# Kernel tuning notes

Hardware: AMD Instinct MI355X
Metric: run time of the kernel (lower is better)

The kernel has to match this reference:

```python
import jax, jax.numpy as jnp
import numpy as np

SIGMA = 1e-4   # SoftRas coverage sharpness
GAMMA = 0.1    # depth-softmax temperature
IMAGE_SIZE = 128


def _normalize(v):
    return v / (jnp.linalg.norm(v, axis=-1, keepdims=True) + 1e-8)


def _look_at(eye, center, up):
    z = _normalize(eye - center)
    x = _normalize(jnp.cross(up, z))
    y = jnp.cross(z, x)
    R = jnp.stack([x, y, z], axis=-2)                       # (B,3,3)
    t = -jnp.einsum('bij,bj->bi', R, eye)
    B = eye.shape[0]
    M = jnp.tile(jnp.eye(4, dtype=eye.dtype), (B, 1, 1))
    M = M.at[:, :3, :3].set(R).at[:, :3, 3].set(t)
    return M


def _perspective(fov_y, aspect, near, far):
    f = 1.0 / np.tan(fov_y / 2.0)
    M = np.zeros((4, 4), np.float32)
    M[0, 0] = f / aspect
    M[1, 1] = f
    M[2, 2] = (far + near) / (near - far)
    M[2, 3] = 2.0 * far * near / (near - far)
    M[3, 2] = -1.0
    return jnp.asarray(M)


def _project(verts_world, eye, center, up):
    B, V, _ = verts_world.shape
    view = _look_at(eye, center, up)
    proj = _perspective(np.deg2rad(60.0), 1.0, 0.1, 10.0)
    M = jnp.einsum('ij,bjk->bik', proj, view)
    vh = jnp.concatenate([verts_world, jnp.ones((B, V, 1), verts_world.dtype)], -1)
    clip = jnp.einsum('bij,bvj->bvi', M, vh)
    return clip[..., :3] / (clip[..., 3:4] + 1e-8)            # (B,V,3) NDC


def _edge_dist(p, a, b):
    # p: (H,W,2); a,b: (B,F,2) -> unsigned point-to-segment distance (B,F,H,W)
    pa = p[None, None] - a[:, :, None, None]                  # (B,F,H,W,2)
    ba = (b - a)[:, :, None, None]                            # (B,F,1,1,2)
    t = jnp.clip(jnp.sum(pa * ba, -1) / (jnp.sum(ba * ba, -1) + 1e-12), 0.0, 1.0)
    d = pa - t[..., None] * ba
    return jnp.sqrt(jnp.sum(d * d, -1) + 1e-12)


def _cross2(u, v):
    return u[..., 0] * v[..., 1] - u[..., 1] * v[..., 0]


def _rasterize(verts_ndc, faces, colors, image_size):
    tri = verts_ndc[:, faces]                                 # (B,F,3,3)
    v2, vz = tri[..., :2], tri[..., 2]                        # (B,F,3,2), (B,F,3)
    xs = (jnp.arange(image_size) + 0.5) / image_size * 2.0 - 1.0
    ys = 1.0 - (jnp.arange(image_size) + 0.5) / image_size * 2.0
    X, Y = jnp.meshgrid(xs, ys, indexing='xy')
    p = jnp.stack([X, Y], -1)                                 # (H,W,2)

    a0, a1, a2 = v2[:, :, 0], v2[:, :, 1], v2[:, :, 2]        # (B,F,2)
    area = _cross2(a1 - a0, a2 - a0)[:, :, None, None]        # (B,F,1,1)
    denom = area + jnp.where(area >= 0, 1e-12, -1e-12)
    w0 = _cross2((a2 - a1)[:, :, None, None], p[None, None] - a1[:, :, None, None])
    w1 = _cross2((a0 - a2)[:, :, None, None], p[None, None] - a2[:, :, None, None])
    w2 = _cross2((a1 - a0)[:, :, None, None], p[None, None] - a0[:, :, None, None])
    b0, b1, b2 = w0 / denom, w1 / denom, w2 / denom           # barycentrics (B,F,H,W)
    inside = (b0 >= 0) & (b1 >= 0) & (b2 >= 0)

    d = jnp.minimum(jnp.minimum(_edge_dist(p, a0, a1), _edge_dist(p, a1, a2)),
                    _edge_dist(p, a2, a0))
    sgn = jnp.where(inside, 1.0, -1.0)
    prob = jax.nn.sigmoid(sgn * d * d / SIGMA)                # soft coverage (B,F,H,W)
    sil = 1.0 - jnp.prod(1.0 - prob, axis=1, keepdims=True)   # (B,1,H,W)

    bc0, bc1, bc2 = (jnp.clip(b0, 0., 1.), jnp.clip(b1, 0., 1.), jnp.clip(b2, 0., 1.))
    s = bc0 + bc1 + bc2 + 1e-8
    zpix = (bc0 * vz[:, :, 0, None, None] + bc1 * vz[:, :, 1, None, None]
            + bc2 * vz[:, :, 2, None, None]) / s
    zn = jnp.clip((1.0 - zpix) * 0.5, 0.0, 1.0)               # 1 = near
    m = jnp.max(zn, axis=1, keepdims=True)
    Dw = prob * jnp.exp((zn - m) / GAMMA)
    w_bg = jnp.exp((0.0 - m) / GAMMA)                         # background (far, black)
    Wn = Dw / (jnp.sum(Dw, axis=1, keepdims=True) + w_bg)     # (B,F,H,W)
    face_col = jnp.mean(colors[:, faces], axis=2)             # (B,F,3)
    rgb = jnp.einsum('bfhw,bfc->bchw', Wn, face_col)          # (B,3,H,W)
    return sil, rgb


def setup_inputs() -> dict:
    key = jax.random.key(0)
    k1, k2, k3, k4 = jax.random.split(key, 4)
    B, V, F = 4, 256, 256
    verts_world = jax.random.normal(k1, (B, V, 3), jnp.float32) * 0.5
    faces = jax.random.randint(k2, (F, 3), 0, V)
    colors = jax.random.uniform(k3, (B, V, 3), jnp.float32)
    eye = jnp.tile(jnp.array([0.0, 0.0, 2.5], jnp.float32), (B, 1)) \
          + jax.random.normal(k4, (B, 3), jnp.float32) * 0.05
    return {"verts_world": verts_world, "faces": faces, "colors": colors, "eye": eye}


def reference(verts_world, faces, colors, eye):
    B = verts_world.shape[0]
    center = jnp.zeros((B, 3), verts_world.dtype)
    up = jnp.tile(jnp.array([0.0, 1.0, 0.0], verts_world.dtype), (B, 1))
    verts_ndc = _project(verts_world, eye, center, up)
    return _rasterize(verts_ndc, faces, colors, IMAGE_SIZE)
```

## Files before the change

### kernel.cpp

```cpp
#include <hip/hip_runtime.h>

#define NB 4
#define NV 256
#define NF 256
#define IMG 128
#define STRIDE 60

typedef float v2f __attribute__((ext_vector_type(2)));

__device__ __forceinline__ float rcpf(float x) { return __builtin_amdgcn_rcpf(x); }
__device__ __forceinline__ float med01(float x) { return __builtin_amdgcn_fmed3f(x, 0.0f, 1.0f); }
__device__ __forceinline__ v2f fma2(v2f a, v2f b, v2f c) { return __builtin_elementwise_fma(a, b, c); }


__global__ void prep_faces(const float* __restrict__ verts,
                           const int* __restrict__ faces,
                           const float* __restrict__ colors,
                           const float* __restrict__ eye,
                           float* __restrict__ fd)
{
    int gid = blockIdx.x * blockDim.x + threadIdx.x;
    if (gid >= NB * NF) return;
    int b = gid >> 8;
    int f = gid & 255;

    const float fpj = 1.7320508075688772f;
    const float p22 = -1.0202020202020203f;
    const float p23 = -0.20202020202020202f;

    float ex = eye[b*3+0], ey = eye[b*3+1], ez = eye[b*3+2];
    float en  = sqrtf(ex*ex + ey*ey + ez*ez);
    float izn = 1.0f / (en + 1e-8f);
    float zx = ex*izn, zy = ey*izn, zz = ez*izn;
    float cn  = sqrtf(zz*zz + zx*zx);
    float ixn = 1.0f / (cn + 1e-8f);
    float xx = zz*ixn, xy = 0.0f, xz = -zx*ixn;
    float yx = zy*xz - zz*xy;
    float yy = zz*xx - zx*xz;
    float yz = zx*xy - zy*xx;
    float tx = -(xx*ex + xy*ey + xz*ez);
    float ty = -(yx*ex + yy*ey + yz*ez);
    float tz = -(zx*ex + zy*ey + zz*ez);

    int i0 = faces[f*3+0], i1 = faces[f*3+1], i2 = faces[f*3+2];
    int idx[3] = { i0, i1, i2 };

    float ax[3], ay[3], az[3];
#pragma unroll
    for (int k = 0; k < 3; ++k) {
        const float* v = verts + (b*NV + idx[k])*3;
        float vx = v[0], vy = v[1], vz = v[2];
        float cx  = fpj*(xx*vx + xy*vy + xz*vz + tx);
        float cyv = fpj*(yx*vx + yy*vy + yz*vz + ty);
        float zv  = zx*vx + zy*vy + zz*vz + tz;
        float cz  = p22*zv + p23;
        float cw  = -zv;
        float iw  = 1.0f / (cw + 1e-8f);
        ax[k] = cx*iw; ay[k] = cyv*iw; az[k] = cz*iw;
    }

    float a0x = ax[0], a0y = ay[0];
    float a1x = ax[1], a1y = ay[1];
    float a2x = ax[2], a2y = ay[2];

    float e01x = a1x - a0x, e01y = a1y - a0y;
    float e12x = a2x - a1x, e12y = a2y - a1y;
    float e20x = a0x - a2x, e20y = a0y - a2y;

    float area  = e01x*(a2y - a0y) - e01y*(a2x - a0x);
    float denom = area + (area >= 0.0f ? 1e-12f : -1e-12f);
    float idn   = 1.0f / denom;

    float A0 = -e12y*idn, B0 = e12x*idn, C0 = (e12y*a1x - e12x*a1y)*idn;
    float A1 = -e20y*idn, B1 = e20x*idn, C1 = (e20y*a2x - e20x*a2y)*idn;
    float A2 = -e01y*idn, B2 = e01x*idn, C2 = (e01y*a0x - e01x*a0y)*idn;

    float ib01 = 1.0f / (e01x*e01x + e01y*e01y + 1e-12f);
    float ib12 = 1.0f / (e12x*e12x + e12y*e12y + 1e-12f);
    float ib20 = 1.0f / (e20x*e20x + e20y*e20y + 1e-12f);

    const float third = (1.0f/3.0f);
    float cr = (colors[(b*NV+i0)*3+0] + colors[(b*NV+i1)*3+0] + colors[(b*NV+i2)*3+0]) * third;
    float cg = (colors[(b*NV+i0)*3+1] + colors[(b*NV+i1)*3+1] + colors[(b*NV+i2)*3+1]) * third;
    float cb = (colors[(b*NV+i0)*3+2] + colors[(b*NV+i1)*3+2] + colors[(b*NV+i2)*3+2]) * third;

    float* o = fd + (b*128 + (f >> 1))*STRIDE + (f & 1);
    o[ 0]=A0;   o[ 2]=B0;   o[ 4]=C0;
    o[ 6]=A1;   o[ 8]=B1;   o[10]=C1;
    o[12]=A2;   o[14]=B2;   o[16]=C2;
    o[18]=a0x;  o[20]=a0y;
    o[22]=e01x; o[24]=e01y; o[26]=e12x; o[28]=e12y; o[30]=e20x; o[32]=e20y;
    o[34]=e01x*ib01; o[36]=e01y*ib01;
    o[38]=e12x*ib12; o[40]=e12y*ib12;
    o[42]=e20x*ib20; o[44]=e20y*ib20;
    o[46]=az[0]; o[48]=az[1]; o[50]=az[2];
    o[52]=cr;   o[54]=cg;   o[56]=cb;
}

__launch_bounds__(512)
__global__ void raster(const float* __restrict__ fd, float* __restrict__ out)
{
    __shared__ float sP[8][64], sS[8][64];
    __shared__ float sR0[8][64], sR1[8][64], sR2[8][64];

    const int t   = threadIdx.x;
    const int cy  = threadIdx.y;
    const int b   = blockIdx.x >> 8;
    const int grp = blockIdx.x & 255;
    const int pixb = grp*64 + t;
    const int h = pixb >> 7;
    const int w = pixb & 127;

    const float px = (w + 0.5f) * (1.0f/64.0f) - 1.0f;
    const float py = 1.0f - (h + 0.5f) * (1.0f/64.0f);
    const v2f px2 = { px, px };
    const v2f py2 = { py, py };

    int foff = (b*128 + cy*16) * STRIDE;
    foff = __builtin_amdgcn_readfirstlane(foff);
    const float* fc = fd + foff;

    const float KSIG = 14426.950408889634f;
    const float KGAM = 14.426950408889634f;
    const v2f KSIG2 = { KSIG, KSIG };
    const v2f KGAM2 = { KGAM, KGAM };
    const v2f ONE2  = { 1.0f, 1.0f };
    const v2f NHALF = { -0.5f, -0.5f };
    const v2f HALF  = { 0.5f, 0.5f };
    const v2f EPS2  = { 1e-8f, 1e-8f };

    v2f prod2 = { 1.0f, 1.0f };
    v2f S2  = { 0.0f, 0.0f };
    v2f R02 = { 0.0f, 0.0f };
    v2f R12 = { 0.0f, 0.0f };
    v2f R22 = { 0.0f, 0.0f };

    for (int i = 0; i < 16; ++i) {
        const float* c = fc + i*STRIDE;
#define LD(k) (*(const v2f*)(c + 2*(k)))
        v2f A0 = LD(0),  B0 = LD(1),  C0 = LD(2);
        v2f A1 = LD(3),  B1 = LD(4),  C1 = LD(5);
        v2f A2 = LD(6),  B2 = LD(7),  C2 = LD(8);
        v2f a0x = LD(9), a0y = LD(10);
        v2f e01x = LD(11), e01y = LD(12);
        v2f e12x = LD(13), e12y = LD(14);
        v2f e20x = LD(15), e20y = LD(16);
        v2f g01x = LD(17), g01y = LD(18);
        v2f g12x = LD(19), g12y = LD(20);
        v2f g20x = LD(21), g20y = LD(22);
        v2f z0 = LD(23), z1 = LD(24), z2 = LD(25);
        v2f cr = LD(26), cg = LD(27), cb = LD(28);
#undef LD

        v2f b0 = fma2(A0, px2, B0*py2) + C0;
        v2f b1 = fma2(A1, px2, B1*py2) + C1;
        v2f b2 = fma2(A2, px2, B2*py2) + C2;

        v2f pa0x = px2 - a0x, pa0y = py2 - a0y;
        v2f pa1x = pa0x - e01x, pa1y = pa0y - e01y;
        v2f pa2x = pa0x + e20x, pa2y = pa0y + e20y;

        v2f tt = fma2(pa0x, g01x, pa0y*g01y);
        tt = (v2f){ med01(tt.x), med01(tt.y) };
        v2f dx = fma2(-tt, e01x, pa0x);
        v2f dy = fma2(-tt, e01y, pa0y);
        v2f dd0 = fma2(dx, dx, dy*dy);
        tt = fma2(pa1x, g12x, pa1y*g12y);
        tt = (v2f){ med01(tt.x), med01(tt.y) };
        dx = fma2(-tt, e12x, pa1x);
        dy = fma2(-tt, e12y, pa1y);
        v2f dd1 = fma2(dx, dx, dy*dy);
        tt = fma2(pa2x, g20x, pa2y*g20y);
        tt = (v2f){ med01(tt.x), med01(tt.y) };
        dx = fma2(-tt, e20x, pa2x);
        dy = fma2(-tt, e20y, pa2y);
        v2f dd2 = fma2(dx, dx, dy*dy);

        float ddl = fminf(fminf(dd0.x, dd1.x), dd2.x);
        float ddh = fminf(fminf(dd0.y, dd1.y), dd2.y);
        v2f ddk = ((v2f){ ddl, ddh }) * KSIG2;

        float inl = fminf(fminf(b0.x, b1.x), b2.x);
        float inh = fminf(fminf(b0.y, b1.y), b2.y);
        float qx = (inl >= 0.0f) ? -ddk.x : ddk.x;
        float qy = (inh >= 0.0f) ? -ddk.y : ddk.y;

        v2f e2 = { exp2f(qx), exp2f(qy) };
        v2f den = e2 + ONE2;
        v2f prob = { rcpf(den.x), rcpf(den.y) };

        prod2 = fma2(-prob, prod2, prod2);

        v2f bc0 = { med01(b0.x), med01(b0.y) };
        v2f bc1 = { med01(b1.x), med01(b1.y) };
        v2f bc2 = { med01(b2.x), med01(b2.y) };
        v2f s   = (bc0 + bc1) + (bc2 + EPS2);
        v2f zs  = fma2(bc0, z0, fma2(bc1, z1, bc2*z2));
        v2f irs = { rcpf(s.x), rcpf(s.y) };
        v2f zp  = zs * irs;
        v2f zn  = fma2(zp, NHALF, HALF);
        zn = (v2f){ med01(zn.x), med01(zn.y) };

        v2f znk = zn * KGAM2;
        v2f ez  = { exp2f(znk.x), exp2f(znk.y) };
        v2f wgt = prob * ez;

        S2  = S2 + wgt;
        R02 = fma2(wgt, cr, R02);
        R12 = fma2(wgt, cg, R12);
        R22 = fma2(wgt, cb, R22);
    }

    sP[cy][t]  = prod2.x * prod2.y;
    sS[cy][t]  = S2.x  + S2.y;
    sR0[cy][t] = R02.x + R02.y;
    sR1[cy][t] = R12.x + R12.y;
    sR2[cy][t] = R22.x + R22.y;
    __syncthreads();

    if (cy == 0) {
        float P  = 1.0f, St = 0.0f, r0 = 0.0f, r1 = 0.0f, r2 = 0.0f;
#pragma unroll
        for (int c2 = 0; c2 < 8; ++c2) {
            P  *= sP[c2][t];
            St += sS[c2][t];
            r0 += sR0[c2][t];
            r1 += sR1[c2][t];
            r2 += sR2[c2][t];
        }
        float iden = rcpf(St + 1.0f);

        out[b*16384 + pixb] = 1.0f - P;
        float* rgb = out + 65536;
        rgb[(b*3 + 0)*16384 + pixb] = r0 * iden;
        rgb[(b*3 + 1)*16384 + pixb] = r1 * iden;
        rgb[(b*3 + 2)*16384 + pixb] = r2 * iden;
    }
}

extern "C" void kernel_launch(void* const* d_in, const int* in_sizes, int n_in,
                              void* d_out, int out_size, void* d_ws, size_t ws_size,
                              hipStream_t stream)
{
    const float* verts  = (const float*)d_in[0];
    const int*   faces  = (const int*)d_in[1];
    const float* colors = (const float*)d_in[2];
    const float* eye    = (const float*)d_in[3];
    float* out = (float*)d_out;
    float* fd  = (float*)d_ws;

    hipLaunchKernelGGL(prep_faces, dim3(4), dim3(256), 0, stream,
                       verts, faces, colors, eye, fd);
    hipLaunchKernelGGL(raster, dim3(1024), dim3(64, 8), 0, stream, fd, out);
}
```

Before: 37.85 us.

## Fold sigma/gamma scaling into face data, use constant-address scalar loads

Prescales the edge and vertex data by sqrt(KSIG) in the prep kernel so the distance comes out already multiplied by the sigma constant, and folds the gamma scale into the depth-normalisation FMA and clamp. The inside test is rewritten as a max of negated barycentrics plus copysign, and the barycentric evaluation becomes a nested FMA. Face data is padded to stride 64 and read through the constant address space so the compiler can use scalar memory loads. It also switches to the raw hardware exp2 and adds unroll 2. Risks are small numerical differences from the prescaling and raw exp2, and changed edge behaviour where a barycentric is exactly zero.

```diff
diff --git a/kernel.cpp b/kernel.cpp
--- a/kernel.cpp
+++ b/kernel.cpp
@@ -4,12 +4,15 @@
 #define NV 256
 #define NF 256
 #define IMG 128
-#define STRIDE 60
+#define STRIDE 64
 
 typedef float v2f __attribute__((ext_vector_type(2)));
+#define CONST_AS __attribute__((address_space(4)))
 
 __device__ __forceinline__ float rcpf(float x) { return __builtin_amdgcn_rcpf(x); }
+__device__ __forceinline__ float ex2(float x)  { return __builtin_amdgcn_exp2f(x); }
 __device__ __forceinline__ float med01(float x) { return __builtin_amdgcn_fmed3f(x, 0.0f, 1.0f); }
+__device__ __forceinline__ v2f med01_2(v2f v) { return (v2f){ med01(v.x), med01(v.y) }; }
 __device__ __forceinline__ v2f fma2(v2f a, v2f b, v2f c) { return __builtin_elementwise_fma(a, b, c); }
 
 
@@ -27,6 +30,8 @@
     const float fpj = 1.7320508075688772f;
     const float p22 = -1.0202020202020203f;
     const float p23 = -0.20202020202020202f;
+    const float SC  = 120.11224139682566f;
+    const float ISC = 1.0f / 120.11224139682566f;
 
     float ex = eye[b*3+0], ey = eye[b*3+1], ez = eye[b*3+2];
     float en  = sqrtf(ex*ex + ey*ey + ez*ez);
@@ -88,11 +93,11 @@
     o[ 0]=A0;   o[ 2]=B0;   o[ 4]=C0;
     o[ 6]=A1;   o[ 8]=B1;   o[10]=C1;
     o[12]=A2;   o[14]=B2;   o[16]=C2;
-    o[18]=a0x;  o[20]=a0y;
-    o[22]=e01x; o[24]=e01y; o[26]=e12x; o[28]=e12y; o[30]=e20x; o[32]=e20y;
-    o[34]=e01x*ib01; o[36]=e01y*ib01;
-    o[38]=e12x*ib12; o[40]=e12y*ib12;
-    o[42]=e20x*ib20; o[44]=e20y*ib20;
+    o[18]=a0x*SC;  o[20]=a0y*SC;
+    o[22]=e01x*SC; o[24]=e01y*SC; o[26]=e12x*SC; o[28]=e12y*SC; o[30]=e20x*SC; o[32]=e20y*SC;
+    o[34]=e01x*ib01*ISC; o[36]=e01y*ib01*ISC;
+    o[38]=e12x*ib12*ISC; o[40]=e12y*ib12*ISC;
+    o[42]=e20x*ib20*ISC; o[44]=e20y*ib20*ISC;
     o[46]=az[0]; o[48]=az[1]; o[50]=az[2];
     o[52]=cr;   o[54]=cg;   o[56]=cb;
 }
@@ -113,21 +118,23 @@
 
     const float px = (w + 0.5f) * (1.0f/64.0f) - 1.0f;
     const float py = 1.0f - (h + 0.5f) * (1.0f/64.0f);
-    const v2f px2 = { px, px };
-    const v2f py2 = { py, py };
+    const float SC = 120.11224139682566f;
+    const v2f px2  = { px, px };
+    const v2f py2  = { py, py };
+    const v2f pxs2 = { px*SC, px*SC };
+    const v2f pys2 = { py*SC, py*SC };
+
+    const float KGAM = 14.426950408889634f;
+    const v2f KGH_NEG = { -0.5f*KGAM, -0.5f*KGAM };
+    const v2f KGH_POS = {  0.5f*KGAM,  0.5f*KGAM };
+    const v2f ONE2 = { 1.0f, 1.0f };
+    const v2f EPS2 = { 1e-8f, 1e-8f };
 
     int foff = (b*128 + cy*16) * STRIDE;
     foff = __builtin_amdgcn_readfirstlane(foff);
-    const float* fc = fd + foff;
-
-    const float KSIG = 14426.950408889634f;
-    const float KGAM = 14.426950408889634f;
-    const v2f KSIG2 = { KSIG, KSIG };
-    const v2f KGAM2 = { KGAM, KGAM };
-    const v2f ONE2  = { 1.0f, 1.0f };
-    const v2f NHALF = { -0.5f, -0.5f };
-    const v2f HALF  = { 0.5f, 0.5f };
-    const v2f EPS2  = { 1e-8f, 1e-8f };
+    const float* fda = (const float*)__builtin_assume_aligned(fd, 256);
+    const CONST_AS float* fc =
+        (const CONST_AS float*)(unsigned long long)(fda + foff);
 
     v2f prod2 = { 1.0f, 1.0f };
     v2f S2  = { 0.0f, 0.0f };
@@ -135,9 +142,10 @@
     v2f R12 = { 0.0f, 0.0f };
     v2f R22 = { 0.0f, 0.0f };
 
+#pragma unroll 2
     for (int i = 0; i < 16; ++i) {
-        const float* c = fc + i*STRIDE;
-#define LD(k) (*(const v2f*)(c + 2*(k)))
+        const CONST_AS float* c = fc + i*STRIDE;
+#define LD(k) (*(const CONST_AS v2f*)(c + 2*(k)))
         v2f A0 = LD(0),  B0 = LD(1),  C0 = LD(2);
         v2f A1 = LD(3),  B1 = LD(4),  C1 = LD(5);
         v2f A2 = LD(6),  B2 = LD(7),  C2 = LD(8);
@@ -152,57 +160,48 @@
         v2f cr = LD(26), cg = LD(27), cb = LD(28);
 #undef LD
 
-        v2f b0 = fma2(A0, px2, B0*py2) + C0;
-        v2f b1 = fma2(A1, px2, B1*py2) + C1;
-        v2f b2 = fma2(A2, px2, B2*py2) + C2;
-
-        v2f pa0x = px2 - a0x, pa0y = py2 - a0y;
+        v2f b0 = fma2(A0, px2, fma2(B0, py2, C0));
+        v2f b1 = fma2(A1, px2, fma2(B1, py2, C1));
+        v2f b2 = fma2(A2, px2, fma2(B2, py2, C2));
+
+        v2f pa0x = pxs2 - a0x, pa0y = pys2 - a0y;
         v2f pa1x = pa0x - e01x, pa1y = pa0y - e01y;
         v2f pa2x = pa0x + e20x, pa2y = pa0y + e20y;
 
-        v2f tt = fma2(pa0x, g01x, pa0y*g01y);
-        tt = (v2f){ med01(tt.x), med01(tt.y) };
+        v2f tt = med01_2(fma2(pa0x, g01x, pa0y*g01y));
         v2f dx = fma2(-tt, e01x, pa0x);
         v2f dy = fma2(-tt, e01y, pa0y);
         v2f dd0 = fma2(dx, dx, dy*dy);
-        tt = fma2(pa1x, g12x, pa1y*g12y);
-        tt = (v2f){ med01(tt.x), med01(tt.y) };
+        tt = med01_2(fma2(pa1x, g12x, pa1y*g12y));
         dx = fma2(-tt, e12x, pa1x);
         dy = fma2(-tt, e12y, pa1y);
         v2f dd1 = fma2(dx, dx, dy*dy);
-        tt = fma2(pa2x, g20x, pa2y*g20y);
-        tt = (v2f){ med01(tt.x), med01(tt.y) };
+        tt = med01_2(fma2(pa2x, g20x, pa2y*g20y));
         dx = fma2(-tt, e20x, pa2x);
         dy = fma2(-tt, e20y, pa2y);
         v2f dd2 = fma2(dx, dx, dy*dy);
 
         float ddl = fminf(fminf(dd0.x, dd1.x), dd2.x);
         float ddh = fminf(fminf(dd0.y, dd1.y), dd2.y);
-        v2f ddk = ((v2f){ ddl, ddh }) * KSIG2;
-
-        float inl = fminf(fminf(b0.x, b1.x), b2.x);
-        float inh = fminf(fminf(b0.y, b1.y), b2.y);
-        float qx = (inl >= 0.0f) ? -ddk.x : ddk.x;
-        float qy = (inh >= 0.0f) ? -ddk.y : ddk.y;
-
-        v2f e2 = { exp2f(qx), exp2f(qy) };
+        float mxl = fmaxf(fmaxf(-b0.x, -b1.x), -b2.x);
+        float mxh = fmaxf(fmaxf(-b0.y, -b1.y), -b2.y);
+        float qx = copysignf(ddl, mxl);
+        float qy = copysignf(ddh, mxh);
+
+        v2f e2  = { ex2(qx), ex2(qy) };
         v2f den = e2 + ONE2;
         v2f prob = { rcpf(den.x), rcpf(den.y) };
 
         prod2 = fma2(-prob, prod2, prod2);
 
-        v2f bc0 = { med01(b0.x), med01(b0.y) };
-        v2f bc1 = { med01(b1.x), med01(b1.y) };
-        v2f bc2 = { med01(b2.x), med01(b2.y) };
+        v2f bc0 = med01_2(b0), bc1 = med01_2(b1), bc2 = med01_2(b2);
         v2f s   = (bc0 + bc1) + (bc2 + EPS2);
         v2f zs  = fma2(bc0, z0, fma2(bc1, z1, bc2*z2));
         v2f irs = { rcpf(s.x), rcpf(s.y) };
-        v2f zp  = zs * irs;
-        v2f zn  = fma2(zp, NHALF, HALF);
-        zn = (v2f){ med01(zn.x), med01(zn.y) };
-
-        v2f znk = zn * KGAM2;
-        v2f ez  = { exp2f(znk.x), exp2f(znk.y) };
+        v2f zq  = fma2(zs*irs, KGH_NEG, KGH_POS);
+        float znx = __builtin_amdgcn_fmed3f(zq.x, 0.0f, KGAM);
+        float zny = __builtin_amdgcn_fmed3f(zq.y, 0.0f, KGAM);
+        v2f ez  = { ex2(znx), ex2(zny) };
         v2f wgt = prob * ez;
 
         S2  = S2 + wgt;
```

After: 35.55 us. 6.1% less time.
